# Performance work log

Hardware: AMD Instinct MI355X
Metric: run time of the kernel (lower is better)

Reference implementation:

```python
import jax, jax.numpy as jnp
import numpy as np

N_NODES = 50000
N_EDGES = 400000
BATCH = 512
D_ENC = 768
HID = 256
LABELS = 4096
LN_EPS = 1e-5
NEG_SLOPE = 0.2  # PyG GATv2 default


def setup_inputs() -> dict:
    key = jax.random.key(0)
    ks = iter(jax.random.split(key, 40))
    f32 = jnp.float32
    def w(shape, scale=0.02):
        return (jax.random.normal(next(ks), shape, dtype=f32) * scale)
    inp = {
        'word_feats': jax.random.normal(next(ks), (BATCH, D_ENC), dtype=f32),
        'gloss_feats': jax.random.normal(next(ks), (N_NODES, D_ENC), dtype=f32),
        'edges': jax.random.randint(next(ks), (2, N_EDGES), 0, N_NODES),
        'labels_size': LABELS,
        # word branch
        'Ww': w((D_ENC, HID)), 'bw': jnp.zeros((HID,), f32),
        'gw1': jnp.ones((HID,), f32), 'bw1': jnp.zeros((HID,), f32),
        # concept branch
        'Wc': w((D_ENC, HID)), 'bc': jnp.zeros((HID,), f32),
        'gc1': jnp.ones((HID,), f32), 'bc1': jnp.zeros((HID,), f32),
        # gat2 (GATv2Conv: lin_l for source, lin_r for target, att vector, out bias)
        'g2_Wl': w((HID, HID)), 'g2_Wr': w((HID, HID)),
        'g2_bl': jnp.zeros((HID,), f32), 'g2_br': jnp.zeros((HID,), f32),
        'g2_att': w((HID,)), 'g2_bias': jnp.zeros((HID,), f32),
        'gc2': jnp.ones((HID,), f32), 'bc2': jnp.zeros((HID,), f32),
        # gat3
        'g3_Wl': w((HID, HID)), 'g3_Wr': w((HID, HID)),
        'g3_bl': jnp.zeros((HID,), f32), 'g3_br': jnp.zeros((HID,), f32),
        'g3_att': w((HID,)), 'g3_bias': jnp.zeros((HID,), f32),
        'gc3': jnp.ones((HID,), f32), 'bc3': jnp.zeros((HID,), f32),
    }
    return inp


def _ln(x, g, b):
    mu = jnp.mean(x, -1, keepdims=True)
    var = jnp.mean((x - mu) ** 2, -1, keepdims=True)
    return (x - mu) * jax.lax.rsqrt(var + LN_EPS) * g + b


def _norm_gelu(x, g, b):
    # LayerNorm -> GELU (exact erf, torch default). Dropout = identity (eval).
    return jax.nn.gelu(_ln(x, g, b), approximate=False)


def _gatv2(x, edges, Wl, Wr, bl, br, att, bias):
    n = x.shape[0]
    loops = jnp.arange(n, dtype=edges.dtype)
    src = jnp.concatenate([edges[0], loops])  # message source j
    dst = jnp.concatenate([edges[1], loops])  # message target i
    xl = x @ Wl + bl  # source transform [N,H]
    xr = x @ Wr + br  # target transform [N,H]
    # e_ij = att . leaky_relu(xl[j] + xr[i])
    e = jnp.sum(att * jax.nn.leaky_relu(xl[src] + xr[dst], NEG_SLOPE), axis=-1)  # [E+N]
    m = jax.ops.segment_max(e, dst, num_segments=n)
    ee = jnp.exp(e - m[dst])
    denom = jax.ops.segment_sum(ee, dst, num_segments=n)
    alpha = ee / denom[dst]
    out = jax.ops.segment_sum(alpha[:, None] * xl[src], dst, num_segments=n)
    return out + bias


def reference(word_feats, gloss_feats, edges, labels_size,
              Ww, bw, gw1, bw1, Wc, bc, gc1, bc1,
              g2_Wl, g2_Wr, g2_bl, g2_br, g2_att, g2_bias, gc2, bc2,
              g3_Wl, g3_Wr, g3_bl, g3_br, g3_att, g3_bias, gc3, bc3):
    refined = _norm_gelu(word_feats @ Ww + bw, gw1, bw1)  # [B, HID]
    g = _norm_gelu(gloss_feats @ Wc + bc, gc1, bc1)  # [N, HID]
    g = _gatv2(g, edges, g2_Wl, g2_Wr, g2_bl, g2_br, g2_att, g2_bias)
    g = _norm_gelu(g, gc2, bc2)
    g = _gatv2(g, edges, g3_Wl, g3_Wr, g3_bl, g3_br, g3_att, g3_bias)
    g = _norm_gelu(g, gc3, bc3)
    gnn_vector = g[:labels_size]
    return refined, gnn_vector
```

## Files before the change

kernel.cpp:

```cpp
#include <hip/hip_runtime.h>
#include <hip/hip_bf16.h>

#define HID 256
#define LN_EPS 1e-5f
#define NEG_SLOPE 0.2f
#define BM 128
#define BN 256
#define BK 32

typedef __attribute__((ext_vector_type(8))) short short8;
typedef __attribute__((ext_vector_type(4))) float f32x4;

__device__ __forceinline__ float gelu_exact(float x){
  return 0.5f*x*(1.0f + erff(x*0.7071067811865476f));
}
__device__ __forceinline__ float lrelu(float x){ return x>0.f ? x : NEG_SLOPE*x; }
__device__ __forceinline__ float wave_sum64(float v){
  #pragma unroll
  for (int o=32;o>0;o>>=1) v += __shfl_xor(v,o,64);
  return v;
}
__device__ __forceinline__ void wave_sum64_x4(float& a, float& b, float& c, float& d){
  #pragma unroll
  for (int o=32;o>0;o>>=1){
    a += __shfl_xor(a,o,64);
    b += __shfl_xor(b,o,64);
    c += __shfl_xor(c,o,64);
    d += __shfl_xor(d,o,64);
  }
}
__device__ __forceinline__ unsigned short f2bf(float x){
  unsigned u = __float_as_uint(x);
  u = (u + 0x7FFFu + ((u>>16)&1u)) >> 16;
  return (unsigned short)u;
}
__device__ __forceinline__ float bf2f(unsigned short u){
  return __uint_as_float(((unsigned)u)<<16);
}
__device__ __forceinline__ void gload_lds16(const void* g, void* l){
  __builtin_amdgcn_global_load_lds((const __attribute__((address_space(1))) unsigned int*)g,
                                   (__attribute__((address_space(3))) unsigned int*)l, 16, 0, 0);
}

__global__ __launch_bounds__(256) void cvt_bf16_k(const float* __restrict__ in,
                                                  unsigned short* __restrict__ out, long n){
  long i = ((long)blockIdx.x*blockDim.x + threadIdx.x)*8;
  const long stride = (long)gridDim.x*blockDim.x*8;
  for (; i < n; i += stride){
    float4 a = *(const float4*)(in+i);
    float4 b = *(const float4*)(in+i+4);
    short8 c;
    c[0]=(short)f2bf(a.x); c[1]=(short)f2bf(a.y); c[2]=(short)f2bf(a.z); c[3]=(short)f2bf(a.w);
    c[4]=(short)f2bf(b.x); c[5]=(short)f2bf(b.y); c[6]=(short)f2bf(b.z); c[7]=(short)f2bf(b.w);
    *(short8*)(out+i) = c;
  }
}

__global__ void edge_hist_k(const int* __restrict__ edges, int* __restrict__ count, int nE, int nN){
  int j = blockIdx.x*blockDim.x + threadIdx.x;
  if (j >= nE+nN) return;
  int dst = (j<nE) ? edges[nE+j] : (j-nE);
  atomicAdd(&count[dst], 1);
}

__global__ __launch_bounds__(256) void scan1_k(const int* __restrict__ count, int* __restrict__ off,
                                               int* __restrict__ bsum, int n, int chunk){
  __shared__ int sh[256];
  const int b = blockIdx.x, t = threadIdx.x;
  const int idx = b*chunk + t;
  int v = (t < chunk && idx < n) ? count[idx] : 0;
  sh[t] = v; __syncthreads();
  int val = v;
  for (int d=1; d<256; d<<=1){
    int tv = (t>=d) ? sh[t-d] : 0;
    __syncthreads();
    val += tv; sh[t] = val;
    __syncthreads();
  }
  if (t < chunk && idx < n) off[idx] = val;
  if (t == 255) bsum[b] = val;
}
__global__ __launch_bounds__(256) void scan2_k(const int* __restrict__ bsum, int* __restrict__ boff,
                                               int* __restrict__ off, int n, int nb){
  __shared__ int sh[256];
  const int t = threadIdx.x;
  int v = (t<nb) ? bsum[t] : 0;
  sh[t] = v; __syncthreads();
  int val = v;
  for (int d=1; d<256; d<<=1){
    int tv = (t>=d) ? sh[t-d] : 0;
    __syncthreads();
    val += tv; sh[t] = val;
    __syncthreads();
  }
  boff[t] = val - v;
  if (t == 255) off[n] = val;
}
__global__ __launch_bounds__(256) void scan3_k(const int* __restrict__ count, const int* __restrict__ boff,
                                               int* __restrict__ off, int n, int chunk){
  const int idx = blockIdx.x*chunk + threadIdx.x;
  if (threadIdx.x < chunk && idx < n)
    off[idx] = off[idx] - count[idx] + boff[blockIdx.x];
}

__global__ void edge_scatter_k(const int* __restrict__ edges, const int* __restrict__ off,
                               int* __restrict__ cursor, int* __restrict__ ssrc, int nE, int nN){
  int j = blockIdx.x*blockDim.x + threadIdx.x;
  if (j >= nE+nN) return;
  int src, dst;
  if (j<nE){ src=edges[j]; dst=edges[nE+j]; } else { src=j-nE; dst=src; }
  int pos = off[dst] + atomicAdd(&cursor[dst],1);
  ssrc[pos]=src;
}

__global__ __launch_bounds__(256) void transpose_bf16_k(const float* __restrict__ in,
                                                        unsigned short* __restrict__ out, int K, int N){
  __shared__ float t[32][33];
  const int kb = blockIdx.x*32, nb = blockIdx.y*32;
  const int tx = threadIdx.x & 31, ty = threadIdx.x >> 5;
  #pragma unroll
  for (int r=ty; r<32; r+=8){
    if (kb+r < K && nb+tx < N) t[r][tx] = in[(long)(kb+r)*N + nb+tx];
  }
  __syncthreads();
  #pragma unroll
  for (int r=ty; r<32; r+=8){
    if (nb+r < N && kb+tx < K) out[(long)(nb+r)*K + kb+tx] = f2bf(t[tx][r]);
  }
}

__global__ __launch_bounds__(256) void word_gemm_ln_gelu_k(
    const float* __restrict__ X, const float* __restrict__ W,
    const float* __restrict__ bias, const float* __restrict__ gamma,
    const float* __restrict__ beta, float* __restrict__ out, int K)
{
  const int tid = threadIdx.x;
  const long row0 = (long)blockIdx.x * 4;
  float acc[4] = {0.f,0.f,0.f,0.f};
  const float* Xb = X + row0*K;
  for (int k=0;k<K;k+=4){
    float w0=W[(long)(k+0)*HID+tid];
    float w1=W[(long)(k+1)*HID+tid];
    float w2=W[(long)(k+2)*HID+tid];
    float w3=W[(long)(k+3)*HID+tid];
    #pragma unroll
    for (int r=0;r<4;r++){
      const float* xp = Xb + (long)r*K + k;
      acc[r] = fmaf(xp[0],w0, fmaf(xp[1],w1, fmaf(xp[2],w2, fmaf(xp[3],w3, acc[r]))));
    }
  }
  __shared__ float red[8];
  const float bv=bias[tid], gv=gamma[tid], btv=beta[tid];
  const int wid=tid>>6, lane=tid&63;
  #pragma unroll
  for (int r=0;r<4;r++){
    float v = acc[r]+bv;
    float p1 = wave_sum64(v), p2 = wave_sum64(v*v);
    __syncthreads();
    if (lane==0){ red[wid]=p1; red[4+wid]=p2; }
    __syncthreads();
    float S1=red[0]+red[1]+red[2]+red[3];
    float S2=red[4]+red[5]+red[6]+red[7];
    float mu = S1*(1.f/HID);
    float var = S2*(1.f/HID) - mu*mu;
    float rs = rsqrtf(var + LN_EPS);
    out[(row0+r)*HID + tid] = gelu_exact((v-mu)*rs*gv + btv);
  }
}

__global__ __launch_bounds__(512) void fused_gloss_proj_k(
    const unsigned short* __restrict__ X, const unsigned short* __restrict__ Wt,
    const float* __restrict__ bc, const float* __restrict__ gc1, const float* __restrict__ bc1,
    const unsigned short* __restrict__ W2,
    const float* __restrict__ bl, const float* __restrict__ br,
    unsigned short* __restrict__ xlr, int M)
{
  constexpr int SLOT1 = BM*BK*2 + BN*BK*2;
  constexpr int B2OFF = 3*SLOT1;
  constexpr int SLOT2 = 256*BK*2;
  __shared__ __align__(16) char lds[B2OFF + 3*SLOT2];
  __shared__ float red_s[BM][4], red_q[BM][4];

  const int tid = threadIdx.x;
  const int wid = tid>>6, lane = tid&63;
  const int wr = wid>>2, wc = wid&3;
  const int lhi = lane>>4, llo = lane&15;
  const long r0 = (long)blockIdx.x * BM;

  {
    f32x4 acc[4][4] = {};
    long ar = r0 + (tid>>2); if (ar > (long)M-1) ar = (long)M-1;
    const unsigned short* gA  = X + ar*768 + (tid&3)*8;
    const unsigned short* gB0 = Wt + (long)(tid>>2)*768 + (tid&3)*8;
    const unsigned short* gB1 = Wt + (long)(128 + (tid>>2))*768 + (tid&3)*8;

    auto stage1 = [&](int s){
      char* b = lds + s*SLOT1;
      gload_lds16(gA,  b + tid*16);         gA  += BK;
      gload_lds16(gB0, b + 8192 + tid*16);  gB0 += BK;
      gload_lds16(gB1, b + 16384 + tid*16); gB1 += BK;
    };
    int offA[4], offB[4];
    #pragma unroll
    for (int m=0;m<4;m++) offA[m] = (wr*64 + m*16 + llo)*64 + lhi*16;
    #pragma unroll
    for (int n=0;n<4;n++) offB[n] = 8192 + (wc*64 + n*16 + llo)*64 + lhi*16;

    stage1(0); stage1(1);
    int cs = 0, ps = 2;
    for (int kt=0; kt<24; ++kt){
      if (kt+1 < 24) asm volatile("s_waitcnt vmcnt(3)" ::: "memory");
      else           asm volatile("s_waitcnt vmcnt(0)" ::: "memory");
      __builtin_amdgcn_s_barrier();
      if (kt+2 < 24) stage1(ps);
      const char* base = lds + cs*SLOT1;
      short8 a[4], b[4];
      #pragma unroll
      for (int m=0;m<4;m++) a[m] = *(const short8*)(base + offA[m]);
      #pragma unroll
      for (int n=0;n<4;n++) b[n] = *(const short8*)(base + offB[n]);
      #pragma unroll
      for (int m=0;m<4;m++)
        #pragma unroll
        for (int n=0;n<4;n++)
          acc[m][n] = __builtin_amdgcn_mfma_f32_16x16x32_bf16(a[m], b[n], acc[m][n], 0,0,0);
      cs = (cs==2)?0:cs+1;
      ps = (ps==2)?0:ps+1;
    }

    const int colb = wc*64 + llo;
    float bv[4], gv[4], btv[4];
    #pragma unroll
    for (int n=0;n<4;n++){ bv[n]=bc[colb+n*16]; gv[n]=gc1[colb+n*16]; btv[n]=bc1[colb+n*16]; }
    __syncthreads();
    #pragma unroll
    for (int m=0;m<4;m++){
      #pragma unroll
      for (int reg=0;reg<4;reg++){
        float s=0.f, q=0.f;
        #pragma unroll
        for (int n=0;n<4;n++){ float v=acc[m][n][reg]+bv[n]; s+=v; q+=v*v; }
        #pragma unroll
        for (int msk=1;msk<16;msk<<=1){ s += __shfl_xor(s,msk,64); q += __shfl_xor(q,msk,64); }
        if (llo==0){ int rl = wr*64+m*16+lhi*4+reg; red_s[rl][wc]=s; red_q[rl][wc]=q; }
      }
    }
    __syncthreads();
    #pragma unroll
    for (int m=0;m<4;m++){
      #pragma unroll
      for (int reg=0;reg<4;reg++){
        int rl = wr*64+m*16+lhi*4+reg;
        float S1 = red_s[rl][0]+red_s[rl][1]+red_s[rl][2]+red_s[rl][3];
        float S2 = red_q[rl][0]+red_q[rl][1]+red_q[rl][2]+red_q[rl][3];
        float mu = S1*(1.f/256.f);
        float var = S2*(1.f/256.f) - mu*mu;
        float rs = rsqrtf(var + LN_EPS);
        #pragma unroll
        for (int n=0;n<4;n++){
          int col = colb + n*16;
          float y = gelu_exact((acc[m][n][reg]+bv[n]-mu)*rs*gv[n] + btv[n]);
          int byte = rl*512 + (((col>>3) ^ (rl&7))<<4) + (col&7)*2;
          *(unsigned short*)(lds + byte) = f2bf(y);
        }
      }
    }
  }
  __syncthreads();

  for (int pass=0; pass<2; ++pass){
    const unsigned short* Wp = W2 + (size_t)pass*256*256;
    const unsigned short* gW0 = Wp + (long)(tid>>2)*256 + (tid&3)*8;
    const unsigned short* gW1 = Wp + (long)(128 + (tid>>2))*256 + (tid&3)*8;
    auto stage2 = [&](int s){
      char* b = lds + B2OFF + s*SLOT2;
      gload_lds16(gW0, b + tid*16);        gW0 += BK;
      gload_lds16(gW1, b + 8192 + tid*16); gW1 += BK;
    };
    f32x4 acc2[4][4] = {};
    __syncthreads();
    stage2(0); stage2(1);
    int cs = 0, ps = 2;
    for (int kt=0; kt<8; ++kt){
      if (kt+1 < 8) asm volatile("s_waitcnt vmcnt(2)" ::: "memory");
      else          asm volatile("s_waitcnt vmcnt(0)" ::: "memory");
      __builtin_amdgcn_s_barrier();
      if (kt+2 < 8) stage2(ps);
      const char* b2base = lds + B2OFF + cs*SLOT2;
      short8 a2[4], b2[4];
      #pragma unroll
      for (int m=0;m<4;m++){
        int row = wr*64 + m*16 + llo;
        int chunk = (kt*4 + lhi) ^ (row&7);
        a2[m] = *(const short8*)(lds + row*512 + chunk*16);
      }
      #pragma unroll
      for (int n=0;n<4;n++) b2[n] = *(const short8*)(b2base + (wc*64 + n*16 + llo)*64 + lhi*16);
      #pragma unroll
      for (int m=0;m<4;m++)
        #pragma unroll
        for (int n=0;n<4;n++)
          acc2[m][n] = __builtin_amdgcn_mfma_f32_16x16x32_bf16(a2[m], b2[n], acc2[m][n], 0,0,0);
      cs = (cs==2)?0:cs+1;
      ps = (ps==2)?0:ps+1;
    }
    const int colb = wc*64 + llo;
    const float* bias = pass ? br : bl;
    float bv[4];
    #pragma unroll
    for (int n=0;n<4;n++) bv[n] = bias[colb + n*16];
    #pragma unroll
    for (int m=0;m<4;m++){
      #pragma unroll
      for (int reg=0;reg<4;reg++){
        long row = r0 + wr*64 + m*16 + lhi*4 + reg;
        if (row < M){
          #pragma unroll
          for (int n=0;n<4;n++)
            xlr[row*512 + pass*256 + colb + n*16] = f2bf(acc2[m][n][reg] + bv[n]);
        }
      }
    }
  }
}

__global__ __launch_bounds__(512) void mfma_gemm_dual_k(
    const unsigned short* __restrict__ X,
    const unsigned short* __restrict__ WtA, const float* __restrict__ biasA,
    unsigned short* __restrict__ outA, int MA, int nblkA,
    const unsigned short* __restrict__ WtB, const float* __restrict__ biasB,
    unsigned short* __restrict__ outB, int MB, int K)
{
  constexpr int ABYTES = BM*BK*2;
  constexpr int SLOT = ABYTES + BN*BK*2;
  __shared__ __align__(16) char lds[3*SLOT];

  const bool jobA = (int)blockIdx.x < nblkA;
  const int bx = jobA ? blockIdx.x : (blockIdx.x - nblkA);
  const unsigned short* Wt = jobA ? WtA : WtB;
  const float* bias = jobA ? biasA : biasB;
  unsigned short* out = jobA ? outA : outB;
  const int M = jobA ? MA : MB;

  const int tid = threadIdx.x;
  const int wid = tid>>6, lane = tid&63;
  const int wr = wid>>2, wc = wid&3;
  const int lhi = lane>>4, llo = lane&15;
  const long r0 = (long)bx * BM;

  f32x4 acc[4][4] = {};

  long ar = r0 + (tid>>2); if (ar > (long)M-1) ar = (long)M-1;
  const unsigned short* gA = X + ar*(long)K + (tid&3)*8;
  const unsigned short* gB0 = Wt + (long)(tid>>2)*K + (tid&3)*8;
  const unsigned short* gB1 = Wt + (long)(128 + (tid>>2))*K + (tid&3)*8;

  auto stage = [&](int s){
    char* base = lds + s*SLOT;
    gload_lds16(gA,  base + tid*16);                 gA  += BK;
    gload_lds16(gB0, base + ABYTES + tid*16);        gB0 += BK;
    gload_lds16(gB1, base + ABYTES + 8192 + tid*16); gB1 += BK;
  };

  int offA[4], offB[4];
  #pragma unroll
  for (int m=0;m<4;m++) offA[m] = (wr*64 + m*16 + llo)*64 + lhi*16;
  #pragma unroll
  for (int n=0;n<4;n++) offB[n] = ABYTES + (wc*64 + n*16 + llo)*64 + lhi*16;

  const int ksteps = K/BK;
  stage(0); stage(1);
  int cs = 0, ps = 2;
  for (int kt=0; kt<ksteps; ++kt){
    if (kt+1 < ksteps) asm volatile("s_waitcnt vmcnt(3)" ::: "memory");
    else               asm volatile("s_waitcnt vmcnt(0)" ::: "memory");
    __builtin_amdgcn_s_barrier();
    if (kt+2 < ksteps) stage(ps);
    const char* base = lds + cs*SLOT;
    short8 a[4], b[4];
    #pragma unroll
    for (int m=0;m<4;m++) a[m] = *(const short8*)(base + offA[m]);
    #pragma unroll
    for (int n=0;n<4;n++) b[n] = *(const short8*)(base + offB[n]);
    #pragma unroll
    for (int m=0;m<4;m++)
      #pragma unroll
      for (int n=0;n<4;n++)
        acc[m][n] = __builtin_amdgcn_mfma_f32_16x16x32_bf16(a[m], b[n], acc[m][n], 0,0,0);
    cs = (cs==2)?0:cs+1;
    ps = (ps==2)?0:ps+1;
  }

  const int colb = wc*64 + llo;
  float bv[4];
  #pragma unroll
  for (int n=0;n<4;n++) bv[n] = bias[colb + n*16];

  #pragma unroll
  for (int m=0;m<4;m++){
    #pragma unroll
    for (int reg=0;reg<4;reg++){
      long row = r0 + wr*64 + m*16 + lhi*4 + reg;
      if (row < M){
        #pragma unroll
        for (int n=0;n<4;n++)
          out[row*256 + colb + n*16] = f2bf(acc[m][n][reg] + bv[n]);
      }
    }
  }
}

template<bool BF16OUT>
__global__ __launch_bounds__(256) void gat_edge_k(
    const unsigned short* __restrict__ xl, int ldl,
    const unsigned short* __restrict__ xr, int ldr,
    const int* __restrict__ off, const int* __restrict__ ssrc,
    const float* __restrict__ att, const float* __restrict__ bias,
    const float* __restrict__ gamma, const float* __restrict__ beta,
    void* __restrict__ gout, int ndst)
{
  const int lane = threadIdx.x & 63;
  const int d = blockIdx.x*4 + (threadIdx.x>>6);
  if (d >= ndst) return;
  const float4 att4 = ((const float4*)att)[lane];
  ushort4 ru = ((const ushort4*)(xr + (size_t)d*ldr))[lane];
  const float rx=bf2f(ru.x), ry=bf2f(ru.y), rz=bf2f(ru.z), rw=bf2f(ru.w);
  const int e0=off[d], e1=off[d+1];
  float m=-1e30f, denom=0.f;
  float4 acc={0.f,0.f,0.f,0.f};

  int i = e0;
  for (; i+4 <= e1; i += 4){
    int s0=ssrc[i], s1=ssrc[i+1], s2=ssrc[i+2], s3=ssrc[i+3];
    ushort4 u0=((const ushort4*)(xl+(size_t)s0*ldl))[lane];
    ushort4 u1=((const ushort4*)(xl+(size_t)s1*ldl))[lane];
    ushort4 u2=((const ushort4*)(xl+(size_t)s2*ldl))[lane];
    ushort4 u3=((const ushort4*)(xl+(size_t)s3*ldl))[lane];
    float a0x=bf2f(u0.x),a0y=bf2f(u0.y),a0z=bf2f(u0.z),a0w=bf2f(u0.w);
    float a1x=bf2f(u1.x),a1y=bf2f(u1.y),a1z=bf2f(u1.z),a1w=bf2f(u1.w);
    float a2x=bf2f(u2.x),a2y=bf2f(u2.y),a2z=bf2f(u2.z),a2w=bf2f(u2.w);
    float a3x=bf2f(u3.x),a3y=bf2f(u3.y),a3z=bf2f(u3.z),a3w=bf2f(u3.w);
    float e0v = att4.x*lrelu(a0x+rx)+att4.y*lrelu(a0y+ry)+att4.z*lrelu(a0z+rz)+att4.w*lrelu(a0w+rw);
    float e1v = att4.x*lrelu(a1x+rx)+att4.y*lrelu(a1y+ry)+att4.z*lrelu(a1z+rz)+att4.w*lrelu(a1w+rw);
    float e2v = att4.x*lrelu(a2x+rx)+att4.y*lrelu(a2y+ry)+att4.z*lrelu(a2z+rz)+att4.w*lrelu(a2w+rw);
    float e3v = att4.x*lrelu(a3x+rx)+att4.y*lrelu(a3y+ry)+att4.z*lrelu(a3z+rz)+att4.w*lrelu(a3w+rw);
    wave_sum64_x4(e0v, e1v, e2v, e3v);
    float bm = fmaxf(fmaxf(e0v,e1v), fmaxf(e2v,e3v));
    if (bm > m){
      float sc = expf(m - bm);
      denom *= sc; acc.x*=sc; acc.y*=sc; acc.z*=sc; acc.w*=sc;
      m = bm;
    }
    float x0=expf(e0v-m), x1=expf(e1v-m), x2=expf(e2v-m), x3=expf(e3v-m);
    denom += x0+x1+x2+x3;
    acc.x += x0*a0x + x1*a1x + x2*a2x + x3*a3x;
    acc.y += x0*a0y + x1*a1y + x2*a2y + x3*a3y;
    acc.z += x0*a0z + x1*a1z + x2*a2z + x3*a3z;
    acc.w += x0*a0w + x1*a1w + x2*a2w + x3*a3w;
  }
  for (; i < e1; ++i){
    int src=ssrc[i];
    ushort4 au = ((const ushort4*)(xl + (size_t)src*ldl))[lane];
    float ax=bf2f(au.x), ay=bf2f(au.y), az=bf2f(au.z), aw=bf2f(au.w);
    float e = att4.x*lrelu(ax+rx)+att4.y*lrelu(ay+ry)
            + att4.z*lrelu(az+rz)+att4.w*lrelu(aw+rw);
    e = wave_sum64(e);
    if (e > m){
      float sc = expf(m - e);
      denom *= sc; acc.x*=sc; acc.y*=sc; acc.z*=sc; acc.w*=sc;
      m = e;
    }
    float ee = expf(e - m);
    denom += ee;
    acc.x += ee*ax; acc.y += ee*ay; acc.z += ee*az; acc.w += ee*aw;
  }

  float inv = 1.0f/denom;
  const float4 b4=((const float4*)bias)[lane];
  float4 o;
  o.x=acc.x*inv+b4.x; o.y=acc.y*inv+b4.y; o.z=acc.z*inv+b4.z; o.w=acc.w*inv+b4.w;
  float S1 = wave_sum64(o.x+o.y+o.z+o.w);
  float S2 = wave_sum64(o.x*o.x+o.y*o.y+o.z*o.z+o.w*o.w);
  float mu=S1*(1.f/256.f);
  float var=S2*(1.f/256.f)-mu*mu;
  float rs=rsqrtf(var+LN_EPS);
  const float4 g4=((const float4*)gamma)[lane];
  const float4 bb4=((const float4*)beta)[lane];
  float4 y;
  y.x=gelu_exact((o.x-mu)*rs*g4.x+bb4.x);
  y.y=gelu_exact((o.y-mu)*rs*g4.y+bb4.y);
  y.z=gelu_exact((o.z-mu)*rs*g4.z+bb4.z);
  y.w=gelu_exact((o.w-mu)*rs*g4.w+bb4.w);
  if constexpr (BF16OUT){
    ushort4 p; p.x=f2bf(y.x); p.y=f2bf(y.y); p.z=f2bf(y.z); p.w=f2bf(y.w);
    ((ushort4*)((unsigned short*)gout + (size_t)d*HID))[lane] = p;
  } else {
    ((float4*)((float*)gout + (size_t)d*HID))[lane] = y;
  }
}

extern "C" void kernel_launch(void* const* d_in, const int* in_sizes, int n_in,
                              void* d_out, int out_size, void* d_ws, size_t ws_size,
                              hipStream_t stream)
{
  const float* word  = (const float*)d_in[0];
  const float* gloss = (const float*)d_in[1];
  const int*   edges = (const int*)d_in[2];
  const float* Ww=(const float*)d_in[4];  const float* bw=(const float*)d_in[5];
  const float* gw1=(const float*)d_in[6]; const float* bw1=(const float*)d_in[7];
  const float* Wc=(const float*)d_in[8];  const float* bc=(const float*)d_in[9];
  const float* gc1=(const float*)d_in[10];const float* bc1=(const float*)d_in[11];
  const float* g2_Wl=(const float*)d_in[12]; const float* g2_Wr=(const float*)d_in[13];
  const float* g2_bl=(const float*)d_in[14]; const float* g2_br=(const float*)d_in[15];
  const float* g2_att=(const float*)d_in[16];const float* g2_bias=(const float*)d_in[17];
  const float* gc2=(const float*)d_in[18];   const float* bc2=(const float*)d_in[19];
  const float* g3_Wl=(const float*)d_in[20]; const float* g3_Wr=(const float*)d_in[21];
  const float* g3_bl=(const float*)d_in[22]; const float* g3_br=(const float*)d_in[23];
  const float* g3_att=(const float*)d_in[24];const float* g3_bias=(const float*)d_in[25];
  const float* gc3=(const float*)d_in[26];   const float* bc3=(const float*)d_in[27];

  const int D  = 768;
  const int nE = in_sizes[2]/2;
  const int nN = in_sizes[1]/D;
  const int B  = in_sizes[0]/D;
  const int E  = nE + nN;
  const int Mpad = (nN + 127) & ~127;
  const int chunk = (nN + 255) / 256;

  char* ws = (char*)d_ws;
  size_t o = 0;
  auto alloc = [&](size_t bytes)->char* { char* p = ws + o; o += (bytes + 255) & ~(size_t)255; return p; };
  int*   off    = (int*)  alloc((size_t)(nN+1)*4);
  int*   count  = (int*)  alloc((size_t)nN*4);
  int*   bsum   = (int*)  alloc(256*4);
  int*   boff   = (int*)  alloc(256*4);
  int*   ssrc   = (int*)  alloc((size_t)E*4);
  unsigned short* WcT = (unsigned short*)alloc((size_t)256*768*2);
  unsigned short* W2T = (unsigned short*)alloc((size_t)512*256*2);
  unsigned short* W3T = (unsigned short*)alloc((size_t)512*256*2);
  char* uni2 = alloc((size_t)nN*D*2);
  unsigned short* glossb = (unsigned short*)uni2;
  unsigned short* Gb     = (unsigned short*)uni2;
  unsigned short* xlr = (unsigned short*)alloc((size_t)nN*512*2);
  unsigned short* xl3 = xlr;
  unsigned short* xr3 = xlr + (size_t)nN*256;

  hipMemsetAsync(count, 0, (size_t)nN*4, stream);
  edge_hist_k<<<(E+255)/256, 256, 0, stream>>>(edges, count, nE, nN);
  scan1_k<<<256, 256, 0, stream>>>(count, off, bsum, nN, chunk);
  scan2_k<<<1, 256, 0, stream>>>(bsum, boff, off, nN, 256);
  scan3_k<<<256, 256, 0, stream>>>(count, boff, off, nN, chunk);
  hipMemsetAsync(count, 0, (size_t)nN*4, stream);
  edge_scatter_k<<<(E+255)/256, 256, 0, stream>>>(edges, off, count, ssrc, nE, nN);

  transpose_bf16_k<<<dim3(24,8),256,0,stream>>>(Wc, WcT, 768,256);
  transpose_bf16_k<<<dim3(8,8),256,0,stream>>>(g2_Wl, W2T, 256,256);
  transpose_bf16_k<<<dim3(8,8),256,0,stream>>>(g2_Wr, W2T + 256*256, 256,256);
  transpose_bf16_k<<<dim3(8,8),256,0,stream>>>(g3_Wl, W3T, 256,256);
  transpose_bf16_k<<<dim3(8,8),256,0,stream>>>(g3_Wr, W3T + 256*256, 256,256);

  cvt_bf16_k<<<2048, 256, 0, stream>>>(gloss, glossb, (long)nN*D);

  float* refined = (float*)d_out;
  float* gnn     = (float*)d_out + (size_t)B*HID;

  word_gemm_ln_gelu_k<<<B/4, 256, 0, stream>>>(word, Ww, bw, gw1, bw1, refined, D);

  fused_gloss_proj_k<<<Mpad/BM, 512, 0, stream>>>(glossb, WcT, bc, gc1, bc1,
                                                  W2T, g2_bl, g2_br, xlr, nN);

  gat_edge_k<true><<<(nN+3)/4,256,0,stream>>>(xlr,512, xlr+256,512, off,ssrc, g2_att,g2_bias,gc2,bc2, Gb, nN);

  mfma_gemm_dual_k<<<Mpad/BM + 4096/BM, 512, 0, stream>>>(
      Gb, W3T, g3_bl, xl3, nN, Mpad/BM,
      W3T + 256*256, g3_br, xr3, 4096, 256);
  gat_edge_k<false><<<4096/4,256,0,stream>>>(xl3,256, xr3,256, off,ssrc, g3_att,g3_bias,gc3,bc3, gnn, 4096);
}
```

Before: 362.9 us.

## Compute layer-3 source projection only for nodes feeding the first 4096 targets

Layer 3's output is only needed for the first 4096 nodes, so the source-side projection xl3 is needed only for nodes that send edges to those targets. The edge scatter now marks such sources, a compaction kernel builds a row map, and the dual GEMM gathers and scatters rows through it, exiting early for blocks past the count. The five weight transposes are also merged into one launch. In exchange it adds a memset, a compaction kernel with atomics, and indirect row access; with random edges roughly 4096*8 sources are marked, so most of the 50k rows are skipped.

```diff
diff --git a/kernel.cpp b/kernel.cpp
--- a/kernel.cpp
+++ b/kernel.cpp
@@ -104,19 +104,38 @@
 }
 
 __global__ void edge_scatter_k(const int* __restrict__ edges, const int* __restrict__ off,
-                               int* __restrict__ cursor, int* __restrict__ ssrc, int nE, int nN){
+                               int* __restrict__ cursor, int* __restrict__ ssrc,
+                               int* __restrict__ mark, int nE, int nN){
   int j = blockIdx.x*blockDim.x + threadIdx.x;
   if (j >= nE+nN) return;
   int src, dst;
   if (j<nE){ src=edges[j]; dst=edges[nE+j]; } else { src=j-nE; dst=src; }
   int pos = off[dst] + atomicAdd(&cursor[dst],1);
   ssrc[pos]=src;
-}
-
-__global__ __launch_bounds__(256) void transpose_bf16_k(const float* __restrict__ in,
-                                                        unsigned short* __restrict__ out, int K, int N){
+  if (dst < 4096) mark[src] = 1;
+}
+
+__global__ void compact_k(const int* __restrict__ mark, int* __restrict__ rowmap,
+                          int* __restrict__ cnt, int n){
+  int i = blockIdx.x*blockDim.x + threadIdx.x;
+  if (i < n && mark[i]) rowmap[atomicAdd(cnt,1)] = i;
+}
+
+__global__ __launch_bounds__(256) void transpose5_k(
+    const float* __restrict__ sWc, unsigned short* __restrict__ dWc,
+    const float* __restrict__ s2l, const float* __restrict__ s2r, unsigned short* __restrict__ dW2,
+    const float* __restrict__ s3l, const float* __restrict__ s3r, unsigned short* __restrict__ dW3)
+{
   __shared__ float t[32][33];
-  const int kb = blockIdx.x*32, nb = blockIdx.y*32;
+  int b = blockIdx.x;
+  const float* in; unsigned short* out; int K, N, kb, nb;
+  if (b < 192){ in=sWc; out=dWc; K=768; N=256; kb=(b%24)*32; nb=(b/24)*32; }
+  else {
+    int j=(b-192)>>6, r=(b-192)&63;
+    K=256; N=256; kb=(r&7)*32; nb=(r>>3)*32;
+    in  = (j==0)?s2l:(j==1)?s2r:(j==2)?s3l:s3r;
+    out = (j==0)?dW2:(j==1)?(dW2+256*256):(j==2)?dW3:(dW3+256*256);
+  }
   const int tx = threadIdx.x & 31, ty = threadIdx.x >> 5;
   #pragma unroll
   for (int r=ty; r<32; r+=8){
@@ -327,7 +346,8 @@
 __global__ __launch_bounds__(512) void mfma_gemm_dual_k(
     const unsigned short* __restrict__ X,
     const unsigned short* __restrict__ WtA, const float* __restrict__ biasA,
-    unsigned short* __restrict__ outA, int MA, int nblkA,
+    unsigned short* __restrict__ outA, const int* __restrict__ rowmapA,
+    const int* __restrict__ cntA, int nblkA,
     const unsigned short* __restrict__ WtB, const float* __restrict__ biasB,
     unsigned short* __restrict__ outB, int MB, int K)
 {
@@ -337,20 +357,24 @@
 
   const bool jobA = (int)blockIdx.x < nblkA;
   const int bx = jobA ? blockIdx.x : (blockIdx.x - nblkA);
+  const long r0 = (long)bx * BM;
+  int Mcap;
+  if (jobA){ Mcap = cntA[0]; if (r0 >= Mcap) return; }
+  else      Mcap = MB;
+
   const unsigned short* Wt = jobA ? WtA : WtB;
   const float* bias = jobA ? biasA : biasB;
   unsigned short* out = jobA ? outA : outB;
-  const int M = jobA ? MA : MB;
 
   const int tid = threadIdx.x;
   const int wid = tid>>6, lane = tid&63;
   const int wr = wid>>2, wc = wid&3;
   const int lhi = lane>>4, llo = lane&15;
-  const long r0 = (long)bx * BM;
 
   f32x4 acc[4][4] = {};
 
-  long ar = r0 + (tid>>2); if (ar > (long)M-1) ar = (long)M-1;
+  long rr = r0 + (tid>>2); if (rr > (long)Mcap-1) rr = Mcap-1;
+  long ar = jobA ? (long)rowmapA[rr] : rr;
   const unsigned short* gA = X + ar*(long)K + (tid&3)*8;
   const unsigned short* gB0 = Wt + (long)(tid>>2)*K + (tid&3)*8;
   const unsigned short* gB1 = Wt + (long)(128 + (tid>>2))*K + (tid&3)*8;
@@ -401,10 +425,11 @@
     #pragma unroll
     for (int reg=0;reg<4;reg++){
       long row = r0 + wr*64 + m*16 + lhi*4 + reg;
-      if (row < M){
+      if (row < Mcap){
+        long orow = jobA ? (long)rowmapA[row] : row;
         #pragma unroll
         for (int n=0;n<4;n++)
-          out[row*256 + colb + n*16] = f2bf(acc[m][n][reg] + bv[n]);
+          out[orow*256 + colb + n*16] = f2bf(acc[m][n][reg] + bv[n]);
       }
     }
   }
@@ -535,6 +560,9 @@
   int*   bsum   = (int*)  alloc(256*4);
   int*   boff   = (int*)  alloc(256*4);
   int*   ssrc   = (int*)  alloc((size_t)E*4);
+  int*   mark   = (int*)  alloc((size_t)(nN+1)*4);
+  int*   cntp   = mark + nN;
+  int*   rowmap = (int*)  alloc((size_t)nN*4);
   unsigned short* WcT = (unsigned short*)alloc((size_t)256*768*2);
   unsigned short* W2T = (unsigned short*)alloc((size_t)512*256*2);
   unsigned short* W3T = (unsigned short*)alloc((size_t)512*256*2);
@@ -546,18 +574,16 @@
   unsigned short* xr3 = xlr + (size_t)nN*256;
 
   hipMemsetAsync(count, 0, (size_t)nN*4, stream);
+  hipMemsetAsync(mark, 0, (size_t)(nN+1)*4, stream);
   edge_hist_k<<<(E+255)/256, 256, 0, stream>>>(edges, count, nE, nN);
   scan1_k<<<256, 256, 0, stream>>>(count, off, bsum, nN, chunk);
   scan2_k<<<1, 256, 0, stream>>>(bsum, boff, off, nN, 256);
   scan3_k<<<256, 256, 0, stream>>>(count, boff, off, nN, chunk);
   hipMemsetAsync(count, 0, (size_t)nN*4, stream);
-  edge_scatter_k<<<(E+255)/256, 256, 0, stream>>>(edges, off, count, ssrc, nE, nN);
-
-  transpose_bf16_k<<<dim3(24,8),256,0,stream>>>(Wc, WcT, 768,256);
-  transpose_bf16_k<<<dim3(8,8),256,0,stream>>>(g2_Wl, W2T, 256,256);
-  transpose_bf16_k<<<dim3(8,8),256,0,stream>>>(g2_Wr, W2T + 256*256, 256,256);
-  transpose_bf16_k<<<dim3(8,8),256,0,stream>>>(g3_Wl, W3T, 256,256);
-  transpose_bf16_k<<<dim3(8,8),256,0,stream>>>(g3_Wr, W3T + 256*256, 256,256);
+  edge_scatter_k<<<(E+255)/256, 256, 0, stream>>>(edges, off, count, ssrc, mark, nE, nN);
+  compact_k<<<(nN+255)/256, 256, 0, stream>>>(mark, rowmap, cntp, nN);
+
+  transpose5_k<<<192 + 4*64, 256, 0, stream>>>(Wc, WcT, g2_Wl, g2_Wr, W2T, g3_Wl, g3_Wr, W3T);
 
   cvt_bf16_k<<<2048, 256, 0, stream>>>(gloss, glossb, (long)nN*D);
 
@@ -572,7 +598,7 @@
   gat_edge_k<true><<<(nN+3)/4,256,0,stream>>>(xlr,512, xlr+256,512, off,ssrc, g2_att,g2_bias,gc2,bc2, Gb, nN);
 
   mfma_gemm_dual_k<<<Mpad/BM + 4096/BM, 512, 0, stream>>>(
-      Gb, W3T, g3_bl, xl3, nN, Mpad/BM,
+      Gb, W3T, g3_bl, xl3, rowmap, cntp, Mpad/BM,
       W3T + 256*256, g3_br, xr3, 4096, 256);
   gat_edge_k<false><<<4096/4,256,0,stream>>>(xl3,256, xr3,256, off,ssrc, g3_att,g3_bias,gc3,bc3, gnn, 4096);
 }
```

Result: slower. 379.8 us (+4.7%).
